# Optimization experiments

Measured on AMD Instinct MI355X. Metric: run time of the kernel, lower is better.

## Reference

```python
import jax, jax.numpy as jnp
import numpy as np

B, N_PER_GRAPH = 16, 512          # uniform graphs -> to_dense_batch is a reshape
N_TOKENS = B * N_PER_GRAPH
M = 32                            # neighbors per node
D_MODEL, D_EDGE, H = 256, 128, 8


def _layernorm(x, g, b, eps=1e-5):
    m = jnp.mean(x, axis=-1, keepdims=True)
    v = jnp.mean((x - m) ** 2, axis=-1, keepdims=True)
    return (x - m) * jax.lax.rsqrt(v + eps) * g + b


def _frame_ops():
    # 2^3 = 8 sign-flip operations, matches FrameAveraging.create_ops
    d = jnp.array([-1.0, 1.0], dtype=jnp.float32)
    g = jnp.meshgrid(d, d, d, indexing='ij')
    return jnp.stack(g, axis=-1).reshape(8, 3)


def _forward(token_embs, geo_feats, edge_feats, neighbor_indices, neighbor_masks,
             ln_qkv_g, ln_qkv_b, W_qkv, b_qkv, ln_e_g, ln_e_b, W_qkv_e, b_qkv_e,
             w_attn, w_edge, W_gate, b_gate, W_fc1, b_fc1, ln_h_g, ln_h_b,
             W_fc2, b_fc2, W_fa, b_fa):
    n = token_embs.shape[0]
    d_head = D_MODEL // H
    de_head = D_EDGE // H
    # qkv transformation
    qkv = _layernorm(token_embs, ln_qkv_g, ln_qkv_b) @ W_qkv + b_qkv
    q, k, v = [a.reshape(n, H, d_head) for a in jnp.split(qkv, 3, axis=-1)]
    qkve = _layernorm(edge_feats, ln_e_g, ln_e_b) @ W_qkv_e + b_qkv_e
    qe, ve = [a.reshape(n, M, H, de_head) for a in jnp.split(qkve, 2, axis=-1)]
    gate = jax.nn.sigmoid(token_embs @ W_gate + b_gate)            # [n,1]
    # GAT-style MLP attention over gathered neighbors
    message = q[:, None] + k[neighbor_indices]                     # [n,M,H,d]
    attn = jnp.einsum('nmhd,d->nmh', message, w_attn) \
         + jnp.einsum('nmhe,e->nmh', qe, w_edge)
    attn = jnp.where(neighbor_masks[..., None], attn, -1e9)
    attn = jax.nn.softmax(jnp.transpose(attn, (0, 2, 1)), axis=-1)  # [n,H,M]
    # context aggregation
    v_n = v[neighbor_indices]                                      # [n,M,H,d]
    scalar_ctx = jnp.einsum('nhm,nmhd->nhd', attn, v_n).reshape(n, -1)
    edge_ctx = jnp.einsum('nhm,nmhd->nhd', attn, ve).reshape(n, -1)
    hcat = jnp.concatenate([scalar_ctx, edge_ctx], axis=-1)
    hmid = _layernorm(jax.nn.gelu(hcat @ W_fc1 + b_fc1, approximate=False), ln_h_g, ln_h_b)
    scalar_out = hmid @ W_fc2 + b_fc2 + token_embs
    # geometric branch with frame averaging (n_heads > 1 path)
    Xb = geo_feats.reshape(B, N_PER_GRAPH, 3)                      # dense batch, full mask
    center = Xb.mean(axis=1)                                       # [B,3]
    Xc = Xb - center[:, None]
    C = jax.lax.stop_gradient(jnp.einsum('bni,bnj->bij', Xc, Xc))  # backward=False -> detach
    _, V = jnp.linalg.eigh(C)                                      # symmetric, UPLO irrelevant
    ops = _frame_ops()
    F_ops = jax.lax.stop_gradient(ops[None, :, None, :] * V[:, None])  # [B,8,3,3]
    h_fr = jnp.einsum('bpj,boji->bopi', Xc, F_ops)                 # [B,8,N,3]
    geo_f = jnp.transpose(h_fr, (1, 0, 2, 3)).reshape(8, n, 3)     # frame-major, node order b*N+p
    geo_neigh = geo_f[:, neighbor_indices]                         # [8,n,M,3]
    geo_ctx = jnp.einsum('nhm,fnmd->fnhd', attn, geo_neigh)        # [8,n,H,3]
    agg = jax.nn.silu(jnp.einsum('fnhd,h->fnd', geo_ctx, W_fa) + b_fa)  # W_frame_agg
    geo_b = jnp.transpose(agg, (1, 0, 2)).reshape(B, N_PER_GRAPH, 8, 3)
    geo_b = jnp.transpose(geo_b, (0, 2, 1, 3))                     # [B,8,N,3]
    inv = jnp.einsum('boij,bopj->bopi', F_ops, geo_b).mean(axis=1) + center[:, None]
    geo_context = inv.reshape(n, 3)
    geo_out = geo_context * gate + geo_feats * (1.0 - gate)
    return scalar_out, geo_out


def setup_inputs() -> dict:
    key = jax.random.key(0)
    ks = jax.random.split(key, 16)
    r = lambda k, shape, s=0.02: (jax.random.normal(k, shape) * s).astype(jnp.float32)
    token_embs = jax.random.normal(ks[0], (N_TOKENS, D_MODEL), dtype=jnp.float32)
    geo_feats = jax.random.normal(ks[1], (N_TOKENS, 3), dtype=jnp.float32)
    edge_feats = jax.random.normal(ks[2], (N_TOKENS, M, D_EDGE), dtype=jnp.float32)
    base = (jnp.arange(N_TOKENS) // N_PER_GRAPH) * N_PER_GRAPH
    neighbor_indices = base[:, None] + jax.random.randint(ks[3], (N_TOKENS, M), 0, N_PER_GRAPH)
    batch_idx = jnp.arange(N_TOKENS) // N_PER_GRAPH
    neighbor_masks = jax.random.uniform(ks[4], (N_TOKENS, M)) < 0.9
    d_head, de_head = D_MODEL // H, D_EDGE // H
    return dict(
        token_embs=token_embs, geo_feats=geo_feats, edge_feats=edge_feats,
        neighbor_indices=neighbor_indices, batch_idx=batch_idx, neighbor_masks=neighbor_masks,
        ln_qkv_g=jnp.ones(D_MODEL), ln_qkv_b=jnp.zeros(D_MODEL),
        W_qkv=r(ks[5], (D_MODEL, 3 * D_MODEL)), b_qkv=jnp.zeros(3 * D_MODEL),
        ln_e_g=jnp.ones(D_EDGE), ln_e_b=jnp.zeros(D_EDGE),
        W_qkv_e=r(ks[6], (D_EDGE, 2 * D_EDGE)), b_qkv_e=jnp.zeros(2 * D_EDGE),
        w_attn=r(ks[7], (d_head,), 0.1), w_edge=r(ks[8], (de_head,), 0.1),
        W_gate=jnp.zeros((D_MODEL, 1)), b_gate=jnp.ones((1,)),   # _init_params
        W_fc1=r(ks[9], (D_MODEL + D_EDGE, D_MODEL)), b_fc1=jnp.zeros(D_MODEL),
        ln_h_g=jnp.ones(D_MODEL), ln_h_b=jnp.zeros(D_MODEL),
        W_fc2=r(ks[10], (D_MODEL, D_MODEL)), b_fc2=jnp.zeros(D_MODEL),
        W_fa=r(ks[11], (H,), 0.3), b_fa=jnp.zeros((1,)),
    )


def reference(token_embs, geo_feats, edge_feats, neighbor_indices, batch_idx, neighbor_masks,
              ln_qkv_g, ln_qkv_b, W_qkv, b_qkv, ln_e_g, ln_e_b, W_qkv_e, b_qkv_e,
              w_attn, w_edge, W_gate, b_gate, W_fc1, b_fc1, ln_h_g, ln_h_b,
              W_fc2, b_fc2, W_fa, b_fa):
    # batch_idx is uniform (arange // N_PER_GRAPH); dense batching handled by reshape
    return _forward(token_embs, geo_feats, edge_feats, neighbor_indices, neighbor_masks,
                    ln_qkv_g, ln_qkv_b, W_qkv, b_qkv, ln_e_g, ln_e_b, W_qkv_e, b_qkv_e,
                    w_attn, w_edge, W_gate, b_gate, W_fc1, b_fc1, ln_h_g, ln_h_b,
                    W_fc2, b_fc2, W_fa, b_fa)
```

## Files before the change

kernel.cpp:

```cpp
#include <hip/hip_runtime.h>
#include <math.h>

#define NTOK 8192
#define NPG  512
#define MNEI 32
#define DM   256
#define DE   128
#define NH   8

#define OFF_WCAT  0u
#define OFF_BCAT  69632u
#define OFF_WEF   69904u
#define OFF_BEF   70928u
#define OFF_FLAG  70936u
#define OFF_QA    70944u
#define OFF_KA    136480u
#define OFF_GATE  202016u
#define OFF_VW    210208u
#define OFF_PROJ  2307360u
#define OFF_VMAT  2331936u
#define OFF_CEN   2332080u
#define OFF_HCAT  2332128u

#define OUT_GEO_OFF 2097152

__device__ __forceinline__ void fma4x4(const float4 a, const float4 w, float4* acc) {
    acc[0].x += a.x*w.x; acc[0].y += a.x*w.y; acc[0].z += a.x*w.z; acc[0].w += a.x*w.w;
    acc[1].x += a.y*w.x; acc[1].y += a.y*w.y; acc[1].z += a.y*w.z; acc[1].w += a.y*w.w;
    acc[2].x += a.z*w.x; acc[2].y += a.z*w.y; acc[2].z += a.z*w.z; acc[2].w += a.z*w.w;
    acc[3].x += a.w*w.x; acc[3].y += a.w*w.y; acc[3].z += a.w*w.z; acc[3].w += a.w*w.w;
}

__global__ __launch_bounds__(256) void k_fold(
    const float* __restrict__ Wqkv, const float* __restrict__ bqkv,
    const float* __restrict__ Wqkve, const float* __restrict__ bqkve,
    const float* __restrict__ w_attn, const float* __restrict__ w_edge,
    const int* __restrict__ maskp, float* __restrict__ ws)
{
    int t = threadIdx.x;
    if (blockIdx.x == 0) {
        __shared__ int sbad, sflt;
        if (t == 0) { sbad = 0; sflt = 0; }
        __syncthreads();
        int bad = 0, flt = 0;
        for (int i = 0; i < 256; i++) {
            unsigned int w = (unsigned int)maskp[i*256 + t];
            if (w > 1u) bad = 1;
            if (w == 0x3F800000u) flt = 1;
        }
        if (bad) atomicOr(&sbad, 1);
        if (flt) atomicOr(&sflt, 1);
        __syncthreads();
        if (t == 0) {
            int f = sflt ? 2 : (sbad ? 1 : 0);
            ((int*)(ws + OFF_FLAG))[0] = f;
        }
        return;
    }
    int gid = (blockIdx.x - 1) * 256 + t;
    if (gid < 69632) {
        int r = gid / 272, c = gid % 272;
        float val;
        if (c < 16) {
            int h = c & 7; int off = (c < 8) ? 0 : 256;
            float s = 0.f;
            for (int d = 0; d < 32; d++) s += Wqkv[r*768 + off + h*32 + d] * w_attn[d];
            val = s;
        } else {
            val = Wqkv[r*768 + 512 + (c - 16)];
        }
        ws[OFF_WCAT + gid] = val;
    } else if (gid < 69632 + 272) {
        int c = gid - 69632;
        float val;
        if (c < 16) {
            int h = c & 7; int off = (c < 8) ? 0 : 256;
            float s = 0.f;
            for (int d = 0; d < 32; d++) s += bqkv[off + h*32 + d] * w_attn[d];
            val = s;
        } else {
            val = bqkv[512 + (c - 16)];
        }
        ws[OFF_BCAT + c] = val;
    } else if (gid < 69904 + 1024) {
        int i = gid - 69904;
        int h = i >> 7, r = i & 127;
        float s = 0.f;
        for (int e = 0; e < 16; e++) s += Wqkve[r*256 + h*16 + e] * w_edge[e];
        ws[OFF_WEF + i] = s;
    } else if (gid < 70928 + 8) {
        int h = gid - 70928;
        float s = 0.f;
        for (int e = 0; e < 16; e++) s += bqkve[h*16 + e] * w_edge[e];
        ws[OFF_BEF + h] = s;
    }
}

__global__ __launch_bounds__(320) void k_tokprep(
    const float* __restrict__ tok, const float* __restrict__ ln_g,
    const float* __restrict__ ln_b, const float* __restrict__ Wgate,
    const float* __restrict__ bgate, float* __restrict__ ws)
{
    __shared__ __align__(16) float sln[256 * 20];
    int t = threadIdx.x;
    int tok0 = blockIdx.x * 16;

    for (int idx = t; idx < 4096; idx += 320) {
        int tt = idx >> 8, k = idx & 255;
        sln[k*20 + tt] = tok[(size_t)(tok0 + tt) * 256 + k];
    }
    __syncthreads();

    int wave = t >> 6, lane = t & 63;
    if (wave < 4) {
        for (int rr = 0; rr < 4; rr++) {
            int tt = wave * 4 + rr;
            float s = 0.f, gdot = 0.f;
            float xs[4];
            for (int q = 0; q < 4; q++) {
                int k = lane + 64*q;
                float x = sln[k*20 + tt];
                xs[q] = x; s += x; gdot += x * Wgate[k];
            }
            for (int m = 32; m >= 1; m >>= 1) { s += __shfl_xor(s,m,64); gdot += __shfl_xor(gdot,m,64); }
            float mu = s * (1.0f/256.0f);
            float vs = 0.f;
            for (int q = 0; q < 4; q++) { float d = xs[q]-mu; vs += d*d; }
            for (int m = 32; m >= 1; m >>= 1) vs += __shfl_xor(vs,m,64);
            float rinv = rsqrtf(vs*(1.0f/256.0f)+1e-5f);
            for (int q = 0; q < 4; q++) {
                int k = lane + 64*q;
                sln[k*20 + tt] = (xs[q]-mu)*rinv*ln_g[k] + ln_b[k];
            }
            if (lane == 0) ws[OFF_GATE + tok0 + tt] = 1.0f/(1.0f+expf(-(gdot + bgate[0])));
        }
    }
    __syncthreads();

    if (t < 272) {
        int i = t / 68, j = t - i*68;
        const float* Wc = ws + OFF_WCAT + 4*j;
        float4 acc[4];
        acc[0] = acc[1] = acc[2] = acc[3] = make_float4(0.f,0.f,0.f,0.f);
        #pragma unroll 4
        for (int k = 0; k < 256; k++) {
            float4 a4 = *(const float4*)&sln[k*20 + 4*i];
            float4 w4 = *(const float4*)&Wc[(size_t)k*272];
            fma4x4(a4, w4, acc);
        }
        float4 b4 = *(const float4*)&ws[OFF_BCAT + 4*j];
        for (int ti = 0; ti < 4; ti++) {
            int n = tok0 + 4*i + ti;
            float4 v = acc[ti];
            v.x += b4.x; v.y += b4.y; v.z += b4.z; v.w += b4.w;
            if (j >= 4) {
                *(float4*)&ws[OFF_VW + (size_t)n*256 + (4*j - 16)] = v;
            } else {
                float vv[4] = {v.x, v.y, v.z, v.w};
                for (int c = 0; c < 4; c++) {
                    int col = 4*j + c;
                    if (col < 8) ws[OFF_QA + n*8 + col] = vv[c];
                    else         ws[OFF_KA + n*8 + (col-8)] = vv[c];
                }
            }
        }
    }
}

__global__ __launch_bounds__(256) void k_geo(const float* __restrict__ geo, float* __restrict__ ws)
{
    __shared__ float sred[4 * 9];
    __shared__ float sres[9];
    __shared__ float sV[9];
    int t = threadIdx.x, g = blockIdx.x;
    int wave = t >> 6, lane = t & 63;
    const float* gp = geo + (size_t)g * NPG * 3;

    float x0[2], y0[2], z0[2];
    float sx = 0.f, sy = 0.f, sz = 0.f;
    for (int i = 0; i < 2; i++) {
        int p = t + 256 * i;
        x0[i] = gp[p*3 + 0]; y0[i] = gp[p*3 + 1]; z0[i] = gp[p*3 + 2];
        sx += x0[i]; sy += y0[i]; sz += z0[i];
    }
    {
        float vals[3] = {sx, sy, sz};
        for (int q = 0; q < 3; q++) {
            float v = vals[q];
            for (int m = 32; m >= 1; m >>= 1) v += __shfl_xor(v, m, 64);
            if (lane == 0) sred[wave*9 + q] = v;
        }
    }
    __syncthreads();
    if (t < 3) {
        float s = 0.f;
        for (int w = 0; w < 4; w++) s += sred[w*9 + t];
        sres[t] = s * (1.0f / 512.0f);
    }
    __syncthreads();
    float cx = sres[0], cy = sres[1], cz = sres[2];

    float c6[6] = {0.f, 0.f, 0.f, 0.f, 0.f, 0.f};
    for (int i = 0; i < 2; i++) {
        float dx = x0[i] - cx, dy = y0[i] - cy, dz = z0[i] - cz;
        c6[0] += dx*dx; c6[1] += dx*dy; c6[2] += dx*dz;
        c6[3] += dy*dy; c6[4] += dy*dz; c6[5] += dz*dz;
    }
    for (int q = 0; q < 6; q++) {
        float v = c6[q];
        for (int m = 32; m >= 1; m >>= 1) v += __shfl_xor(v, m, 64);
        if (lane == 0) sred[wave*9 + q] = v;
    }
    __syncthreads();
    if (t < 6) {
        float s = 0.f;
        for (int w = 0; w < 4; w++) s += sred[w*9 + t];
        sres[t] = s;
    }
    __syncthreads();

    if (t == 0) {
        double a[3][3];
        a[0][0] = sres[0]; a[0][1] = a[1][0] = sres[1]; a[0][2] = a[2][0] = sres[2];
        a[1][1] = sres[3]; a[1][2] = a[2][1] = sres[4]; a[2][2] = sres[5];
        double v[3][3] = {{1,0,0},{0,1,0},{0,0,1}};
        const int ps[3] = {0, 0, 1}, qs[3] = {1, 2, 2};
        for (int sweep = 0; sweep < 10; sweep++) {
            for (int pi = 0; pi < 3; pi++) {
                int p = ps[pi], q = qs[pi];
                double apq = a[p][q];
                if (fabs(apq) < 1e-300) continue;
                double theta = (a[q][q] - a[p][p]) / (2.0 * apq);
                double tt = ((theta >= 0.0) ? 1.0 : -1.0) / (fabs(theta) + sqrt(theta*theta + 1.0));
                double c = 1.0 / sqrt(tt*tt + 1.0), s = tt * c;
                int k = 3 - p - q;
                double app = a[p][p], aqq = a[q][q], akp = a[k][p], akq = a[k][q];
                a[p][p] = app - tt * apq;
                a[q][q] = aqq + tt * apq;
                a[p][q] = 0.0; a[q][p] = 0.0;
                a[k][p] = c*akp - s*akq; a[p][k] = a[k][p];
                a[k][q] = s*akp + c*akq; a[q][k] = a[k][q];
                for (int kk = 0; kk < 3; kk++) {
                    double vp = v[kk][p], vq = v[kk][q];
                    v[kk][p] = c*vp - s*vq;
                    v[kk][q] = s*vp + c*vq;
                }
            }
        }
        for (int r = 0; r < 3; r++)
            for (int c2 = 0; c2 < 3; c2++) {
                float fv = (float)v[r][c2];
                sV[r*3 + c2] = fv;
                ws[OFF_VMAT + g*9 + r*3 + c2] = fv;
            }
        ws[OFF_CEN + g*3 + 0] = cx;
        ws[OFF_CEN + g*3 + 1] = cy;
        ws[OFF_CEN + g*3 + 2] = cz;
    }
    __syncthreads();

    for (int i = 0; i < 2; i++) {
        int p = t + 256 * i;
        float dx = x0[i] - cx, dy = y0[i] - cy, dz = z0[i] - cz;
        for (int c = 0; c < 3; c++) {
            float pr = dx * sV[0*3 + c] + dy * sV[1*3 + c] + dz * sV[2*3 + c];
            ws[OFF_PROJ + (size_t)(g*NPG + p)*3 + c] = pr;
        }
    }
}

__global__ __launch_bounds__(256) void k_attn(
    const float* __restrict__ edge, const int* __restrict__ nbr,
    const void* __restrict__ maskp,
    const float* __restrict__ lneg, const float* __restrict__ lneb,
    const float* __restrict__ bqkve, const float* __restrict__ Wqkve,
    const float* __restrict__ Wfa, const float* __restrict__ bfa,
    const float* __restrict__ geo, float* __restrict__ ws, float* __restrict__ out)
{
    __shared__ __align__(16) float se[32 * 132];
    __shared__ __align__(16) float swe[8 * 132];
    __shared__ float slog[264];
    __shared__ float sattn[264];
    __shared__ int   snbr[32];
    __shared__ int   smask[32];
    __shared__ float swm[32];
    __shared__ float sqa[8], sbef[8];
    __shared__ float sge[128], sbe[128];
    __shared__ float sg3[4];

    int t = threadIdx.x;
    int n = blockIdx.x;
    int g = n >> 9;
    int flag = ((const int*)(ws + OFF_FLAG))[0];

    if (t < 32) {
        snbr[t] = nbr[n*32 + t];
        int mv;
        if (flag == 1)      mv = (int)((const unsigned char*)maskp)[n*32 + t];
        else if (flag == 2) mv = (((const float*)maskp)[n*32 + t] != 0.0f) ? 1 : 0;
        else                mv = ((const int*)maskp)[n*32 + t];
        smask[t] = mv;
    }
    if (t < 8) { sqa[t] = ws[OFF_QA + n*8 + t]; sbef[t] = ws[OFF_BEF + t]; }
    if (t >= 32 && t < 160) { sge[t - 32] = lneg[t - 32]; sbe[t - 32] = lneb[t - 32]; }
    {
        const float* wef = ws + OFF_WEF;
        for (int i = 0; i < 4; i++) {
            int idx = t*4 + i;
            int h = idx >> 7, r = idx & 127;
            swe[h*132 + r] = wef[idx];
        }
    }
    {
        const float4* ep = (const float4*)(edge + (size_t)n * 4096);
        for (int j = 0; j < 4; j++) {
            int l = j*1024 + t*4;
            float4 v4 = ep[l >> 2];
            int m = l >> 7, r = l & 127;
            *(float4*)&se[m*132 + r] = v4;
        }
    }
    __syncthreads();

    {
        int m = t >> 3, sub = t & 7;
        int base = m*132 + sub*16;
        float4 x0 = *(float4*)&se[base + 0];
        float4 x1 = *(float4*)&se[base + 4];
        float4 x2 = *(float4*)&se[base + 8];
        float4 x3 = *(float4*)&se[base + 12];
        float s = x0.x+x0.y+x0.z+x0.w + x1.x+x1.y+x1.z+x1.w
                + x2.x+x2.y+x2.z+x2.w + x3.x+x3.y+x3.z+x3.w;
        for (int mm = 4; mm >= 1; mm >>= 1) s += __shfl_xor(s, mm, 8);
        float mu = s * (1.0f / 128.0f);
        float vs = (x0.x-mu)*(x0.x-mu) + (x0.y-mu)*(x0.y-mu) + (x0.z-mu)*(x0.z-mu) + (x0.w-mu)*(x0.w-mu)
                 + (x1.x-mu)*(x1.x-mu) + (x1.y-mu)*(x1.y-mu) + (x1.z-mu)*(x1.z-mu) + (x1.w-mu)*(x1.w-mu)
                 + (x2.x-mu)*(x2.x-mu) + (x2.y-mu)*(x2.y-mu) + (x2.z-mu)*(x2.z-mu) + (x2.w-mu)*(x2.w-mu)
                 + (x3.x-mu)*(x3.x-mu) + (x3.y-mu)*(x3.y-mu) + (x3.z-mu)*(x3.z-mu) + (x3.w-mu)*(x3.w-mu);
        for (int mm = 4; mm >= 1; mm >>= 1) vs += __shfl_xor(vs, mm, 8);
        float rinv = rsqrtf(vs * (1.0f / 128.0f) + 1e-5f);
        int r0 = sub * 16;
        x0.x = (x0.x-mu)*rinv*sge[r0+0]  + sbe[r0+0];  x0.y = (x0.y-mu)*rinv*sge[r0+1]  + sbe[r0+1];
        x0.z = (x0.z-mu)*rinv*sge[r0+2]  + sbe[r0+2];  x0.w = (x0.w-mu)*rinv*sge[r0+3]  + sbe[r0+3];
        x1.x = (x1.x-mu)*rinv*sge[r0+4]  + sbe[r0+4];  x1.y = (x1.y-mu)*rinv*sge[r0+5]  + sbe[r0+5];
        x1.z = (x1.z-mu)*rinv*sge[r0+6]  + sbe[r0+6];  x1.w = (x1.w-mu)*rinv*sge[r0+7]  + sbe[r0+7];
        x2.x = (x2.x-mu)*rinv*sge[r0+8]  + sbe[r0+8];  x2.y = (x2.y-mu)*rinv*sge[r0+9]  + sbe[r0+9];
        x2.z = (x2.z-mu)*rinv*sge[r0+10] + sbe[r0+10]; x2.w = (x2.w-mu)*rinv*sge[r0+11] + sbe[r0+11];
        x3.x = (x3.x-mu)*rinv*sge[r0+12] + sbe[r0+12]; x3.y = (x3.y-mu)*rinv*sge[r0+13] + sbe[r0+13];
        x3.z = (x3.z-mu)*rinv*sge[r0+14] + sbe[r0+14]; x3.w = (x3.w-mu)*rinv*sge[r0+15] + sbe[r0+15];
        *(float4*)&se[base + 0]  = x0;
        *(float4*)&se[base + 4]  = x1;
        *(float4*)&se[base + 8]  = x2;
        *(float4*)&se[base + 12] = x3;
    }
    __syncthreads();

    {
        int m = t >> 3, h = t & 7;
        float acc = sbef[h];
        #pragma unroll 8
        for (int r = 0; r < 128; r += 4) {
            float4 e4 = *(float4*)&se[m*132 + r];
            float4 w4 = *(float4*)&swe[h*132 + r];
            acc += e4.x*w4.x + e4.y*w4.y + e4.z*w4.z + e4.w*w4.w;
        }
        float lg = sqa[h] + ws[OFF_KA + snbr[m]*8 + h] + acc;
        if (!smask[m]) lg = -1e9f;
        slog[h*33 + m] = lg;
    }
    __syncthreads();

    {
        int h = t >> 5, m = t & 31;
        float x = slog[h*33 + m];
        float mx = x;
        for (int mm = 16; mm >= 1; mm >>= 1) mx = fmaxf(mx, __shfl_xor(mx, mm, 32));
        float e = expf(x - mx);
        float sum = e;
        for (int mm = 16; mm >= 1; mm >>= 1) sum += __shfl_xor(sum, mm, 32);
        sattn[h*33 + m] = e / sum;
    }
    __syncthreads();

    {
        int h = t >> 5;
        float acc = 0.f;
        const float* vw = ws + OFF_VW;
        #pragma unroll 8
        for (int m = 0; m < 32; m++) {
            int row = snbr[m];
            acc += sattn[h*33 + m] * vw[(size_t)row*256 + t];
        }
        ws[OFF_HCAT + (size_t)n*384 + t] = acc;
    }
    {
        int h = t >> 5, rq = (t & 31) * 4;
        float4 acc = make_float4(0.f,0.f,0.f,0.f);
        #pragma unroll 8
        for (int m = 0; m < 32; m++) {
            float a = sattn[h*33 + m];
            float4 e4 = *(float4*)&se[m*132 + rq];
            acc.x += a*e4.x; acc.y += a*e4.y; acc.z += a*e4.z; acc.w += a*e4.w;
        }
        *(float4*)&swe[h*132 + rq] = acc;
    }
    if (t < 32) {
        float acc = 0.f;
        for (int h = 0; h < 8; h++) acc += Wfa[h] * sattn[h*33 + t];
        swm[t] = acc;
    }
    __syncthreads();

    float accEC;
    {
        int col = t & 127, half = t >> 7;
        int h2 = col >> 4;
        int rbase = half * 64;
        const float* wq = Wqkve + 128 + col;
        float a0 = 0.f;
        #pragma unroll 8
        for (int r = 0; r < 64; r++)
            a0 += swe[h2*132 + rbase + r] * wq[(size_t)(rbase + r)*256];
        accEC = a0;
        if (half) slog[col] = a0;
    }
    if (t >= 128 && t < 224) {
        int idx = t - 128;
        int m = idx / 3, c = idx - m*3;
        slog[128 + idx] = swm[m] * ws[OFF_PROJ + (size_t)snbr[m]*3 + c];
    }
    __syncthreads();

    if (t < 128) {
        float tot = accEC + slog[t] + bqkve[128 + t];
        ws[OFF_HCAT + (size_t)n*384 + 256 + t] = tot;
    }
    if (t < 3) {
        float sd = 0.f;
        for (int m = 0; m < 32; m++) sd += slog[128 + m*3 + t];
        float bb = bfa[0];
        float p1 = sd + bb, p2 = -sd + bb;
        float s1v = p1 / (1.0f + expf(-p1));
        float s2v = p2 / (1.0f + expf(-p2));
        sg3[t] = 0.5f * (s1v - s2v);
    }
    __syncthreads();

    if (t < 3) {
        const float* Vm = ws + OFF_VMAT + g*9;
        float gc = Vm[t*3+0]*sg3[0] + Vm[t*3+1]*sg3[1] + Vm[t*3+2]*sg3[2] + ws[OFF_CEN + g*3 + t];
        float gt = ws[OFF_GATE + n];
        out[OUT_GEO_OFF + (size_t)n*3 + t] = gc * gt + geo[(size_t)n*3 + t] * (1.0f - gt);
    }
}

__global__ __launch_bounds__(256) void k_mlp(
    const float* __restrict__ tok, const float* __restrict__ Wfc1,
    const float* __restrict__ bfc1, const float* __restrict__ lnhg,
    const float* __restrict__ lnhb, const float* __restrict__ Wfc2,
    const float* __restrict__ bfc2, const float* __restrict__ ws,
    float* __restrict__ out)
{
    __shared__ __align__(16) float A[384 * 20];
    int t = threadIdx.x;
    int tok0 = blockIdx.x * 16;
    int i = t >> 6, j = t & 63;
    const float* hc = ws + OFF_HCAT;

    for (int it = 0; it < 24; it++) {
        int idx = it*256 + t;
        int tt = idx / 384;
        int k  = idx - tt*384;
        A[k*20 + tt] = hc[(size_t)tok0*384 + idx];
    }
    __syncthreads();

    float4 acc1[4];
    acc1[0] = acc1[1] = acc1[2] = acc1[3] = make_float4(0.f,0.f,0.f,0.f);
    {
        const float* wp = Wfc1 + 4*j;
        #pragma unroll 4
        for (int k = 0; k < 384; k++) {
            float4 a4 = *(const float4*)&A[k*20 + 4*i];
            float4 w4 = *(const float4*)&wp[(size_t)k*256];
            fma4x4(a4, w4, acc1);
        }
    }
    float h[4][4];
    {
        float4 b4 = *(const float4*)&bfc1[4*j];
        for (int ti = 0; ti < 4; ti++) {
            float xv[4] = {acc1[ti].x + b4.x, acc1[ti].y + b4.y, acc1[ti].z + b4.z, acc1[ti].w + b4.w};
            for (int c = 0; c < 4; c++) {
                float x = xv[c];
                h[ti][c] = 0.5f * x * (1.0f + erff(x * 0.70710678118654752f));
            }
        }
    }
    __syncthreads();

    {
        float s[4], q[4];
        for (int ti = 0; ti < 4; ti++) {
            s[ti] = h[ti][0] + h[ti][1] + h[ti][2] + h[ti][3];
            q[ti] = h[ti][0]*h[ti][0] + h[ti][1]*h[ti][1] + h[ti][2]*h[ti][2] + h[ti][3]*h[ti][3];
        }
        for (int m = 32; m >= 1; m >>= 1)
            for (int ti = 0; ti < 4; ti++) {
                s[ti] += __shfl_xor(s[ti], m, 64);
                q[ti] += __shfl_xor(q[ti], m, 64);
            }
        float4 g4 = *(const float4*)&lnhg[4*j];
        float4 b4 = *(const float4*)&lnhb[4*j];
        float gg[4] = {g4.x, g4.y, g4.z, g4.w};
        float bb[4] = {b4.x, b4.y, b4.z, b4.w};
        for (int ti = 0; ti < 4; ti++) {
            float mu = s[ti] * (1.0f/256.0f);
            float var = q[ti] * (1.0f/256.0f) - mu*mu;
            float rinv = rsqrtf(var + 1e-5f);
            for (int c = 0; c < 4; c++) {
                float hn = (h[ti][c] - mu) * rinv * gg[c] + bb[c];
                A[(4*j + c)*20 + 4*i + ti] = hn;
            }
        }
    }
    __syncthreads();

    float4 acc2[4];
    acc2[0] = acc2[1] = acc2[2] = acc2[3] = make_float4(0.f,0.f,0.f,0.f);
    {
        const float* wp = Wfc2 + 4*j;
        #pragma unroll 4
        for (int k = 0; k < 256; k++) {
            float4 a4 = *(const float4*)&A[k*20 + 4*i];
            float4 w4 = *(const float4*)&wp[(size_t)k*256];
            fma4x4(a4, w4, acc2);
        }
    }
    {
        float4 b4 = *(const float4*)&bfc2[4*j];
        for (int ti = 0; ti < 4; ti++) {
            size_t o = (size_t)(tok0 + 4*i + ti) * 256 + 4*j;
            float4 r4 = *(const float4*)&tok[o];
            float4 v;
            v.x = acc2[ti].x + b4.x + r4.x;
            v.y = acc2[ti].y + b4.y + r4.y;
            v.z = acc2[ti].z + b4.z + r4.z;
            v.w = acc2[ti].w + b4.w + r4.w;
            *(float4*)&out[o] = v;
        }
    }
}

extern "C" void kernel_launch(void* const* d_in, const int* in_sizes, int n_in,
                              void* d_out, int out_size, void* d_ws, size_t ws_size,
                              hipStream_t stream) {
    (void)in_sizes; (void)n_in; (void)out_size; (void)ws_size;
    const float* tok   = (const float*)d_in[0];
    const float* geo   = (const float*)d_in[1];
    const float* edge  = (const float*)d_in[2];
    const int*   nbr   = (const int*)d_in[3];
    const void*  maskp = d_in[5];
    const float* ln_qkv_g = (const float*)d_in[6];
    const float* ln_qkv_b = (const float*)d_in[7];
    const float* Wqkv  = (const float*)d_in[8];
    const float* bqkv  = (const float*)d_in[9];
    const float* ln_e_g = (const float*)d_in[10];
    const float* ln_e_b = (const float*)d_in[11];
    const float* Wqkve = (const float*)d_in[12];
    const float* bqkve = (const float*)d_in[13];
    const float* w_attn = (const float*)d_in[14];
    const float* w_edge = (const float*)d_in[15];
    const float* Wgate = (const float*)d_in[16];
    const float* bgate = (const float*)d_in[17];
    const float* Wfc1  = (const float*)d_in[18];
    const float* bfc1  = (const float*)d_in[19];
    const float* lnhg  = (const float*)d_in[20];
    const float* lnhb  = (const float*)d_in[21];
    const float* Wfc2  = (const float*)d_in[22];
    const float* bfc2  = (const float*)d_in[23];
    const float* Wfa   = (const float*)d_in[24];
    const float* bfa   = (const float*)d_in[25];
    float* ws  = (float*)d_ws;
    float* out = (float*)d_out;

    k_fold<<<dim3(279), dim3(256), 0, stream>>>(Wqkv, bqkv, Wqkve, bqkve, w_attn, w_edge,
                                                (const int*)maskp, ws);
    k_tokprep<<<dim3(512), dim3(320), 0, stream>>>(tok, ln_qkv_g, ln_qkv_b, Wgate, bgate, ws);
    k_geo<<<dim3(16), dim3(256), 0, stream>>>(geo, ws);
    k_attn<<<dim3(8192), dim3(256), 0, stream>>>(edge, nbr, maskp, ln_e_g, ln_e_b, bqkve,
                                                 Wqkve, Wfa, bfa, geo, ws, out);
    k_mlp<<<dim3(512), dim3(256), 0, stream>>>(tok, Wfc1, bfc1, lnhg, lnhb, Wfc2, bfc2, ws, out);
}
```

Baseline: 441.6 us.

## Restructure attention kernel: register-resident edge LN, shuffle-reduced logits, fewer barriers

The edge attention kernel now loads edge features straight into registers, applies the layernorm there with gamma and beta read directly from global memory, and computes the per-head edge logits with an 8-lane shuffle reduction. The staged copies of edge features and edge weights, plus one synchronisation point, are gone. The frame-averaging projection sum moves to a wave-level shuffle reduction, which removes another barrier and shared buffer. Attention weights are cached in registers before the aggregation loops. These changes cut shared-memory traffic and barriers per node, in exchange for more registers per thread and more redundant global weight loads.

```diff
diff --git a/kernel.cpp b/kernel.cpp
--- a/kernel.cpp
+++ b/kernel.cpp
@@ -29,6 +29,10 @@
     acc[1].x += a.y*w.x; acc[1].y += a.y*w.y; acc[1].z += a.y*w.z; acc[1].w += a.y*w.w;
     acc[2].x += a.z*w.x; acc[2].y += a.z*w.y; acc[2].z += a.z*w.z; acc[2].w += a.z*w.w;
     acc[3].x += a.w*w.x; acc[3].y += a.w*w.y; acc[3].z += a.w*w.z; acc[3].w += a.w*w.w;
+}
+
+__device__ __forceinline__ float dot4(const float4 a, const float4 b) {
+    return a.x*b.x + a.y*b.y + a.z*b.z + a.w*b.w;
 }
 
 __global__ __launch_bounds__(256) void k_fold(
@@ -278,14 +282,12 @@
     const float* __restrict__ geo, float* __restrict__ ws, float* __restrict__ out)
 {
     __shared__ __align__(16) float se[32 * 132];
-    __shared__ __align__(16) float swe[8 * 132];
-    __shared__ float slog[264];
-    __shared__ float sattn[264];
+    __shared__ __align__(16) float sew[8 * 132];
+    __shared__ __align__(16) float sattn[8 * 36];
+    __shared__ float sbuf[128];
     __shared__ int   snbr[32];
     __shared__ int   smask[32];
-    __shared__ float swm[32];
     __shared__ float sqa[8], sbef[8];
-    __shared__ float sge[128], sbe[128];
     __shared__ float sg3[4];
 
     int t = threadIdx.x;
@@ -302,33 +304,14 @@
         smask[t] = mv;
     }
     if (t < 8) { sqa[t] = ws[OFF_QA + n*8 + t]; sbef[t] = ws[OFF_BEF + t]; }
-    if (t >= 32 && t < 160) { sge[t - 32] = lneg[t - 32]; sbe[t - 32] = lneb[t - 32]; }
-    {
-        const float* wef = ws + OFF_WEF;
-        for (int i = 0; i < 4; i++) {
-            int idx = t*4 + i;
-            int h = idx >> 7, r = idx & 127;
-            swe[h*132 + r] = wef[idx];
-        }
-    }
-    {
-        const float4* ep = (const float4*)(edge + (size_t)n * 4096);
-        for (int j = 0; j < 4; j++) {
-            int l = j*1024 + t*4;
-            float4 v4 = ep[l >> 2];
-            int m = l >> 7, r = l & 127;
-            *(float4*)&se[m*132 + r] = v4;
-        }
-    }
-    __syncthreads();
-
-    {
-        int m = t >> 3, sub = t & 7;
-        int base = m*132 + sub*16;
-        float4 x0 = *(float4*)&se[base + 0];
-        float4 x1 = *(float4*)&se[base + 4];
-        float4 x2 = *(float4*)&se[base + 8];
-        float4 x3 = *(float4*)&se[base + 12];
+
+    int m = t >> 3, sub = t & 7;
+    float4 x0, x1, x2, x3;
+    {
+        const float4* ep = (const float4*)(edge + (size_t)n*4096 + m*128 + sub*16);
+        x0 = ep[0]; x1 = ep[1]; x2 = ep[2]; x3 = ep[3];
+    }
+    {
         float s = x0.x+x0.y+x0.z+x0.w + x1.x+x1.y+x1.z+x1.w
                 + x2.x+x2.y+x2.z+x2.w + x3.x+x3.y+x3.z+x3.w;
         for (int mm = 4; mm >= 1; mm >>= 1) s += __shfl_xor(s, mm, 8);
@@ -339,75 +322,110 @@
                  + (x3.x-mu)*(x3.x-mu) + (x3.y-mu)*(x3.y-mu) + (x3.z-mu)*(x3.z-mu) + (x3.w-mu)*(x3.w-mu);
         for (int mm = 4; mm >= 1; mm >>= 1) vs += __shfl_xor(vs, mm, 8);
         float rinv = rsqrtf(vs * (1.0f / 128.0f) + 1e-5f);
-        int r0 = sub * 16;
-        x0.x = (x0.x-mu)*rinv*sge[r0+0]  + sbe[r0+0];  x0.y = (x0.y-mu)*rinv*sge[r0+1]  + sbe[r0+1];
-        x0.z = (x0.z-mu)*rinv*sge[r0+2]  + sbe[r0+2];  x0.w = (x0.w-mu)*rinv*sge[r0+3]  + sbe[r0+3];
-        x1.x = (x1.x-mu)*rinv*sge[r0+4]  + sbe[r0+4];  x1.y = (x1.y-mu)*rinv*sge[r0+5]  + sbe[r0+5];
-        x1.z = (x1.z-mu)*rinv*sge[r0+6]  + sbe[r0+6];  x1.w = (x1.w-mu)*rinv*sge[r0+7]  + sbe[r0+7];
-        x2.x = (x2.x-mu)*rinv*sge[r0+8]  + sbe[r0+8];  x2.y = (x2.y-mu)*rinv*sge[r0+9]  + sbe[r0+9];
-        x2.z = (x2.z-mu)*rinv*sge[r0+10] + sbe[r0+10]; x2.w = (x2.w-mu)*rinv*sge[r0+11] + sbe[r0+11];
-        x3.x = (x3.x-mu)*rinv*sge[r0+12] + sbe[r0+12]; x3.y = (x3.y-mu)*rinv*sge[r0+13] + sbe[r0+13];
-        x3.z = (x3.z-mu)*rinv*sge[r0+14] + sbe[r0+14]; x3.w = (x3.w-mu)*rinv*sge[r0+15] + sbe[r0+15];
+        const float4* gp4 = (const float4*)(lneg + sub*16);
+        const float4* bp4 = (const float4*)(lneb + sub*16);
+        float4 g0 = gp4[0], g1 = gp4[1], g2 = gp4[2], g3 = gp4[3];
+        float4 b0 = bp4[0], b1 = bp4[1], b2 = bp4[2], b3 = bp4[3];
+        x0.x=(x0.x-mu)*rinv*g0.x+b0.x; x0.y=(x0.y-mu)*rinv*g0.y+b0.y;
+        x0.z=(x0.z-mu)*rinv*g0.z+b0.z; x0.w=(x0.w-mu)*rinv*g0.w+b0.w;
+        x1.x=(x1.x-mu)*rinv*g1.x+b1.x; x1.y=(x1.y-mu)*rinv*g1.y+b1.y;
+        x1.z=(x1.z-mu)*rinv*g1.z+b1.z; x1.w=(x1.w-mu)*rinv*g1.w+b1.w;
+        x2.x=(x2.x-mu)*rinv*g2.x+b2.x; x2.y=(x2.y-mu)*rinv*g2.y+b2.y;
+        x2.z=(x2.z-mu)*rinv*g2.z+b2.z; x2.w=(x2.w-mu)*rinv*g2.w+b2.w;
+        x3.x=(x3.x-mu)*rinv*g3.x+b3.x; x3.y=(x3.y-mu)*rinv*g3.y+b3.y;
+        x3.z=(x3.z-mu)*rinv*g3.z+b3.z; x3.w=(x3.w-mu)*rinv*g3.w+b3.w;
+    }
+    {
+        int base = m*132 + sub*16;
         *(float4*)&se[base + 0]  = x0;
         *(float4*)&se[base + 4]  = x1;
         *(float4*)&se[base + 8]  = x2;
         *(float4*)&se[base + 12] = x3;
     }
-    __syncthreads();
-
-    {
-        int m = t >> 3, h = t & 7;
-        float acc = sbef[h];
-        #pragma unroll 8
-        for (int r = 0; r < 128; r += 4) {
-            float4 e4 = *(float4*)&se[m*132 + r];
-            float4 w4 = *(float4*)&swe[h*132 + r];
-            acc += e4.x*w4.x + e4.y*w4.y + e4.z*w4.z + e4.w*w4.w;
-        }
-        float lg = sqa[h] + ws[OFF_KA + snbr[m]*8 + h] + acc;
+    float acc[8];
+    {
+        const float* wef = ws + OFF_WEF + sub*16;
+        #pragma unroll
+        for (int h = 0; h < 8; h++) {
+            const float4* wp = (const float4*)(wef + h*128);
+            float4 w0 = wp[0], w1 = wp[1], w2 = wp[2], w3 = wp[3];
+            acc[h] = dot4(x0,w0) + dot4(x1,w1) + dot4(x2,w2) + dot4(x3,w3);
+        }
+        #pragma unroll
+        for (int st = 1; st < 8; st <<= 1) {
+            #pragma unroll
+            for (int h = 0; h < 8; h++) acc[h] += __shfl_xor(acc[h], st, 8);
+        }
+    }
+    __syncthreads();
+
+    {
+        float myacc = acc[0];
+        #pragma unroll
+        for (int h = 1; h < 8; h++) myacc = (sub == h) ? acc[h] : myacc;
+        float lg = sqa[sub] + sbef[sub] + myacc + ws[OFF_KA + snbr[m]*8 + sub];
         if (!smask[m]) lg = -1e9f;
-        slog[h*33 + m] = lg;
-    }
-    __syncthreads();
-
-    {
-        int h = t >> 5, m = t & 31;
-        float x = slog[h*33 + m];
+        sattn[sub*36 + m] = lg;
+    }
+    __syncthreads();
+
+    {
+        int h = t >> 5, mm2 = t & 31;
+        float x = sattn[h*36 + mm2];
         float mx = x;
         for (int mm = 16; mm >= 1; mm >>= 1) mx = fmaxf(mx, __shfl_xor(mx, mm, 32));
         float e = expf(x - mx);
         float sum = e;
         for (int mm = 16; mm >= 1; mm >>= 1) sum += __shfl_xor(sum, mm, 32);
-        sattn[h*33 + m] = e / sum;
+        sattn[h*36 + mm2] = e / sum;
     }
     __syncthreads();
 
     {
         int h = t >> 5;
-        float acc = 0.f;
+        float av[32];
+        #pragma unroll
+        for (int k = 0; k < 8; k++) *(float4*)&av[4*k] = *(const float4*)&sattn[h*36 + 4*k];
+
+        float accS = 0.f;
         const float* vw = ws + OFF_VW;
-        #pragma unroll 8
-        for (int m = 0; m < 32; m++) {
-            int row = snbr[m];
-            acc += sattn[h*33 + m] * vw[(size_t)row*256 + t];
-        }
-        ws[OFF_HCAT + (size_t)n*384 + t] = acc;
-    }
-    {
-        int h = t >> 5, rq = (t & 31) * 4;
-        float4 acc = make_float4(0.f,0.f,0.f,0.f);
-        #pragma unroll 8
-        for (int m = 0; m < 32; m++) {
-            float a = sattn[h*33 + m];
-            float4 e4 = *(float4*)&se[m*132 + rq];
-            acc.x += a*e4.x; acc.y += a*e4.y; acc.z += a*e4.z; acc.w += a*e4.w;
-        }
-        *(float4*)&swe[h*132 + rq] = acc;
+        #pragma unroll
+        for (int mm2 = 0; mm2 < 32; mm2++) {
+            int row = snbr[mm2];
+            accS += av[mm2] * vw[(size_t)row*256 + t];
+        }
+        ws[OFF_HCAT + (size_t)n*384 + t] = accS;
+
+        int rq = t & 31;
+        float4 eacc = make_float4(0.f,0.f,0.f,0.f);
+        #pragma unroll
+        for (int mm2 = 0; mm2 < 32; mm2++) {
+            float a = av[mm2];
+            float4 e4 = *(const float4*)&se[mm2*132 + rq*4];
+            eacc.x += a*e4.x; eacc.y += a*e4.y; eacc.z += a*e4.z; eacc.w += a*e4.w;
+        }
+        *(float4*)&sew[h*132 + rq*4] = eacc;
     }
     if (t < 32) {
-        float acc = 0.f;
-        for (int h = 0; h < 8; h++) acc += Wfa[h] * sattn[h*33 + t];
-        swm[t] = acc;
+        float wmv = 0.f;
+        #pragma unroll
+        for (int h2 = 0; h2 < 8; h2++) wmv += Wfa[h2] * sattn[h2*36 + t];
+        int row = snbr[t];
+        const float* pp = ws + OFF_PROJ + (size_t)row*3;
+        float q0 = wmv * pp[0], q1 = wmv * pp[1], q2 = wmv * pp[2];
+        for (int st = 16; st >= 1; st >>= 1) {
+            q0 += __shfl_xor(q0, st, 32);
+            q1 += __shfl_xor(q1, st, 32);
+            q2 += __shfl_xor(q2, st, 32);
+        }
+        if (t < 3) {
+            float sd = (t == 0) ? q0 : (t == 1) ? q1 : q2;
+            float bb = bfa[0];
+            float p1 = sd + bb, p2 = -sd + bb;
+            float s1v = p1 / (1.0f + expf(-p1));
+            float s2v = p2 / (1.0f + expf(-p2));
+            sg3[t] = 0.5f * (s1v - s2v);
+        }
     }
     __syncthreads();
 
@@ -418,34 +436,23 @@
         int rbase = half * 64;
         const float* wq = Wqkve + 128 + col;
         float a0 = 0.f;
-        #pragma unroll 8
-        for (int r = 0; r < 64; r++)
-            a0 += swe[h2*132 + rbase + r] * wq[(size_t)(rbase + r)*256];
+        #pragma unroll
+        for (int k = 0; k < 16; k++) {
+            int r = rbase + 4*k;
+            float4 s4 = *(const float4*)&sew[h2*132 + r];
+            a0 += s4.x * wq[(size_t)(r+0)*256]
+                + s4.y * wq[(size_t)(r+1)*256]
+                + s4.z * wq[(size_t)(r+2)*256]
+                + s4.w * wq[(size_t)(r+3)*256];
+        }
         accEC = a0;
-        if (half) slog[col] = a0;
-    }
-    if (t >= 128 && t < 224) {
-        int idx = t - 128;
-        int m = idx / 3, c = idx - m*3;
-        slog[128 + idx] = swm[m] * ws[OFF_PROJ + (size_t)snbr[m]*3 + c];
+        if (half) sbuf[col] = a0;
     }
     __syncthreads();
 
     if (t < 128) {
-        float tot = accEC + slog[t] + bqkve[128 + t];
-        ws[OFF_HCAT + (size_t)n*384 + 256 + t] = tot;
-    }
-    if (t < 3) {
-        float sd = 0.f;
-        for (int m = 0; m < 32; m++) sd += slog[128 + m*3 + t];
-        float bb = bfa[0];
-        float p1 = sd + bb, p2 = -sd + bb;
-        float s1v = p1 / (1.0f + expf(-p1));
-        float s2v = p2 / (1.0f + expf(-p2));
-        sg3[t] = 0.5f * (s1v - s2v);
-    }
-    __syncthreads();
-
+        ws[OFF_HCAT + (size_t)n*384 + 256 + t] = accEC + sbuf[t] + bqkve[128 + t];
+    }
     if (t < 3) {
         const float* Vm = ws + OFF_VMAT + g*9;
         float gc = Vm[t*3+0]*sg3[0] + Vm[t*3+1]*sg3[1] + Vm[t*3+2]*sg3[2] + ws[OFF_CEN + g*3 + t];
```

Measured after the change: 468.8 us. 6.1% more time.

## Rework attention aggregation in k_attn with float4 gathers and warp-specialized work split

Applied to the files above, without the earlier changes.

Restructures the post-softmax part of k_attn. Half the block gathers neighbor value rows with float4 loads, split over two halves of the neighbors and combined in shared memory. The other half computes the attention-weighted edge context for two heads per thread. The edge-projection matvec now uses float4 weight loads across 8 row groups with a shared-memory reduction, and the frame-averaging sum uses warp shuffles, which removes one barrier stage. The aim is fewer memory instructions and better thread utilisation, at the cost of more shared memory and an extra cross-group reduction.

```diff
diff --git a/kernel.cpp b/kernel.cpp
--- a/kernel.cpp
+++ b/kernel.cpp
@@ -279,11 +279,11 @@
 {
     __shared__ __align__(16) float se[32 * 132];
     __shared__ __align__(16) float swe[8 * 132];
-    __shared__ float slog[264];
-    __shared__ float sattn[264];
+    __shared__ __align__(16) float sew[8 * 132];
+    __shared__ __align__(16) float sattn[8 * 36];
+    __shared__ __align__(16) float sq[64 * 4];
     __shared__ int   snbr[32];
     __shared__ int   smask[32];
-    __shared__ float swm[32];
     __shared__ float sqa[8], sbef[8];
     __shared__ float sge[128], sbe[128];
     __shared__ float sg3[4];
@@ -304,12 +304,9 @@
     if (t < 8) { sqa[t] = ws[OFF_QA + n*8 + t]; sbef[t] = ws[OFF_BEF + t]; }
     if (t >= 32 && t < 160) { sge[t - 32] = lneg[t - 32]; sbe[t - 32] = lneb[t - 32]; }
     {
-        const float* wef = ws + OFF_WEF;
-        for (int i = 0; i < 4; i++) {
-            int idx = t*4 + i;
-            int h = idx >> 7, r = idx & 127;
-            swe[h*132 + r] = wef[idx];
-        }
+        int idx = t * 4;
+        int h = idx >> 7, r = idx & 127;
+        *(float4*)&swe[h*132 + r] = *(const float4*)&ws[OFF_WEF + idx];
     }
     {
         const float4* ep = (const float4*)(edge + (size_t)n * 4096);
@@ -364,88 +361,112 @@
             float4 w4 = *(float4*)&swe[h*132 + r];
             acc += e4.x*w4.x + e4.y*w4.y + e4.z*w4.z + e4.w*w4.w;
         }
-        float lg = sqa[h] + ws[OFF_KA + snbr[m]*8 + h] + acc;
+        float lg = sqa[h] + acc + ws[OFF_KA + snbr[m]*8 + h];
         if (!smask[m]) lg = -1e9f;
-        slog[h*33 + m] = lg;
-    }
-    __syncthreads();
-
-    {
-        int h = t >> 5, m = t & 31;
-        float x = slog[h*33 + m];
+        sattn[h*36 + m] = lg;
+    }
+    __syncthreads();
+
+    {
+        int h = t >> 5, m2 = t & 31;
+        float x = sattn[h*36 + m2];
         float mx = x;
         for (int mm = 16; mm >= 1; mm >>= 1) mx = fmaxf(mx, __shfl_xor(mx, mm, 32));
         float e = expf(x - mx);
         float sum = e;
         for (int mm = 16; mm >= 1; mm >>= 1) sum += __shfl_xor(sum, mm, 32);
-        sattn[h*33 + m] = e / sum;
-    }
-    __syncthreads();
-
-    {
-        int h = t >> 5;
-        float acc = 0.f;
+        sattn[h*36 + m2] = e / sum;
+    }
+    __syncthreads();
+
+    float4 accS = make_float4(0.f,0.f,0.f,0.f);
+    if (t < 128) {
+        int half = t >> 6, c4 = t & 63;
+        int h = c4 >> 3;
         const float* vw = ws + OFF_VW;
-        #pragma unroll 8
-        for (int m = 0; m < 32; m++) {
+        #pragma unroll 4
+        for (int mi = 0; mi < 16; mi++) {
+            int m = half*16 + mi;
+            float a = sattn[h*36 + m];
             int row = snbr[m];
-            acc += sattn[h*33 + m] * vw[(size_t)row*256 + t];
-        }
-        ws[OFF_HCAT + (size_t)n*384 + t] = acc;
-    }
-    {
-        int h = t >> 5, rq = (t & 31) * 4;
-        float4 acc = make_float4(0.f,0.f,0.f,0.f);
-        #pragma unroll 8
-        for (int m = 0; m < 32; m++) {
-            float a = sattn[h*33 + m];
-            float4 e4 = *(float4*)&se[m*132 + rq];
-            acc.x += a*e4.x; acc.y += a*e4.y; acc.z += a*e4.z; acc.w += a*e4.w;
-        }
-        *(float4*)&swe[h*132 + rq] = acc;
-    }
-    if (t < 32) {
-        float acc = 0.f;
-        for (int h = 0; h < 8; h++) acc += Wfa[h] * sattn[h*33 + t];
-        swm[t] = acc;
-    }
-    __syncthreads();
-
-    float accEC;
-    {
-        int col = t & 127, half = t >> 7;
-        int h2 = col >> 4;
-        int rbase = half * 64;
-        const float* wq = Wqkve + 128 + col;
-        float a0 = 0.f;
-        #pragma unroll 8
-        for (int r = 0; r < 64; r++)
-            a0 += swe[h2*132 + rbase + r] * wq[(size_t)(rbase + r)*256];
-        accEC = a0;
-        if (half) slog[col] = a0;
-    }
-    if (t >= 128 && t < 224) {
-        int idx = t - 128;
-        int m = idx / 3, c = idx - m*3;
-        slog[128 + idx] = swm[m] * ws[OFF_PROJ + (size_t)snbr[m]*3 + c];
+            float4 v4 = *(const float4*)&vw[(size_t)row*256 + 4*c4];
+            accS.x += a*v4.x; accS.y += a*v4.y; accS.z += a*v4.z; accS.w += a*v4.w;
+        }
+        if (half) *(float4*)&sq[c4*4] = accS;
+        if (t < 32) {
+            float wmv = 0.f;
+            #pragma unroll
+            for (int h2 = 0; h2 < 8; h2++) wmv += Wfa[h2] * sattn[h2*36 + t];
+            int row = snbr[t];
+            const float* pp = ws + OFF_PROJ + (size_t)row*3;
+            float q0 = wmv * pp[0], q1 = wmv * pp[1], q2 = wmv * pp[2];
+            for (int st = 16; st >= 1; st >>= 1) {
+                q0 += __shfl_xor(q0, st, 32);
+                q1 += __shfl_xor(q1, st, 32);
+                q2 += __shfl_xor(q2, st, 32);
+            }
+            if (t < 3) {
+                float sd = (t == 0) ? q0 : (t == 1) ? q1 : q2;
+                float bb = bfa[0];
+                float p1 = sd + bb, p2 = -sd + bb;
+                float s1v = p1 / (1.0f + expf(-p1));
+                float s2v = p2 / (1.0f + expf(-p2));
+                sg3[t] = 0.5f * (s1v - s2v);
+            }
+        }
+    } else {
+        int rq = t & 31, hb = (t >> 5) - 4;
+        float4 e1 = make_float4(0.f,0.f,0.f,0.f);
+        float4 e2 = make_float4(0.f,0.f,0.f,0.f);
+        #pragma unroll
+        for (int mq = 0; mq < 8; mq++) {
+            float4 a4a = *(const float4*)&sattn[hb*36 + 4*mq];
+            float4 a4b = *(const float4*)&sattn[(hb+4)*36 + 4*mq];
+            float aa[4] = {a4a.x, a4a.y, a4a.z, a4a.w};
+            float ab[4] = {a4b.x, a4b.y, a4b.z, a4b.w};
+            #pragma unroll
+            for (int c = 0; c < 4; c++) {
+                int m = 4*mq + c;
+                float4 e4 = *(const float4*)&se[m*132 + rq*4];
+                e1.x += aa[c]*e4.x; e1.y += aa[c]*e4.y; e1.z += aa[c]*e4.z; e1.w += aa[c]*e4.w;
+                e2.x += ab[c]*e4.x; e2.y += ab[c]*e4.y; e2.z += ab[c]*e4.z; e2.w += ab[c]*e4.w;
+            }
+        }
+        *(float4*)&sew[hb*132 + rq*4]     = e1;
+        *(float4*)&sew[(hb+4)*132 + rq*4] = e2;
+    }
+    __syncthreads();
+
+    float* sec = se;
+    float4 accE = make_float4(0.f,0.f,0.f,0.f);
+    {
+        int col4 = t & 31, rgrp = t >> 5;
+        int h2 = col4 >> 2;
+        const float* wqb = Wqkve + 128 + 4*col4;
+        #pragma unroll 4
+        for (int ri = 0; ri < 16; ri++) {
+            int r = rgrp*16 + ri;
+            float sv = sew[h2*132 + r];
+            float4 w4 = *(const float4*)&wqb[(size_t)r*256];
+            accE.x += sv*w4.x; accE.y += sv*w4.y; accE.z += sv*w4.z; accE.w += sv*w4.w;
+        }
+        if (t < 64) {
+            float4 p = *(const float4*)&sq[t*4];
+            float4 tot;
+            tot.x = accS.x + p.x; tot.y = accS.y + p.y;
+            tot.z = accS.z + p.z; tot.w = accS.w + p.w;
+            *(float4*)&ws[OFF_HCAT + (size_t)n*384 + 4*t] = tot;
+        }
+        *(float4*)&sec[rgrp*128 + col4*4] = accE;
     }
     __syncthreads();
 
     if (t < 128) {
-        float tot = accEC + slog[t] + bqkve[128 + t];
-        ws[OFF_HCAT + (size_t)n*384 + 256 + t] = tot;
-    }
-    if (t < 3) {
-        float sd = 0.f;
-        for (int m = 0; m < 32; m++) sd += slog[128 + m*3 + t];
-        float bb = bfa[0];
-        float p1 = sd + bb, p2 = -sd + bb;
-        float s1v = p1 / (1.0f + expf(-p1));
-        float s2v = p2 / (1.0f + expf(-p2));
-        sg3[t] = 0.5f * (s1v - s2v);
-    }
-    __syncthreads();
-
+        float ec = bqkve[128 + t];
+        #pragma unroll
+        for (int g2 = 0; g2 < 8; g2++) ec += sec[g2*128 + t];
+        ws[OFF_HCAT + (size_t)n*384 + 256 + t] = ec;
+    }
     if (t < 3) {
         const float* Vm = ws + OFF_VMAT + g*9;
         float gc = Vm[t*3+0]*sg3[0] + Vm[t*3+1]*sg3[1] + Vm[t*3+2]*sg3[2] + ws[OFF_CEN + g*3 + t];
```

Result: no change. 437.7 us (-0.9%).
